# Performance work log

Hardware: AMD Instinct MI355X
Metric: run time of the kernel (lower is better)

Reference implementation:

```python
import jax, jax.numpy as jnp
import numpy as np

HID = 512; HH = HID // 2; INP = 1; OUT = 1
INH = int(HID * 0.3); EXC = HID - INH            # 153 / 359
N = 3 * HH + 2 * HID + INP                       # 1793 total units
ALM_EXC_START = 3 * HH + HID                      # start of ALM excitatory block
T_CONST = 0.1; SIGMA_REC = 0.01
B, T = 128, 300


def _np_masks():
    rng = np.random.default_rng(0)
    n_zeros = int(np.ceil(0.9 * HH))
    sparse = np.ones((HH, HH), np.float32)
    for c in range(HH):
        sparse[rng.permutation(HH)[:n_zeros], c] = 0.0
    alm2str = np.concatenate([np.ones((HH, EXC), np.float32), np.zeros((HH, INH), np.float32)], 1)
    thal2d1 = np.concatenate([np.ones((HH // 2, HID), np.float32), np.zeros((HH // 2, HID), np.float32)], 0)
    alm2d1 = 1.0 - thal2d1
    iti2d1 = np.concatenate([np.ones((HH // 2, INP), np.float32), np.zeros((HH // 2, INP), np.float32)], 0)
    alm_sign = np.concatenate([np.ones(EXC, np.float32), -np.ones(INH, np.float32)])  # alm2alm_D diagonal
    return sparse, alm2str, thal2d1, alm2d1, iti2d1, alm_sign

_SPARSE, _ALM2STR, _THAL2D1M, _ALM2D1M, _ITI2D1M, _ALMSIGN = [jnp.asarray(a) for a in _np_masks()]


def _clip(w):
    return jnp.clip(w, 1e-10, 1.0)               # F.hardtanh(w, 1e-10, 1)


def _build_W(d12d1_w, d12d2_w, d22d1_w, d22d2_w, d22stn_w, d12thal_w, stn2thal_w,
             thal2alm_w, alm2alm_w, thal2d1_w, thal2d2_w, alm2d1_w, alm2d2_w,
             inp_w_d1, inp_w_d2):
    z_ss = jnp.zeros((HH, HH)); z_sl = jnp.zeros((HH, HID))
    z_ls = jnp.zeros((HID, HH)); z_ll = jnp.zeros((HID, HID))
    z_si = jnp.zeros((HH, INP)); z_li = jnp.zeros((HID, INP))
    # striatal recurrence: sparse_mask * hardtanh(w) @ (-I)
    d12d1 = -(_SPARSE * _clip(d12d1_w)); d12d2 = -(_SPARSE * _clip(d12d2_w))
    d22d1 = -(_SPARSE * _clip(d22d1_w)); d22d2 = -(_SPARSE * _clip(d22d2_w))
    row_d1 = jnp.concatenate([d12d1, d22d1, z_ss, _THAL2D1M * _clip(thal2d1_w),
                              _ALM2D1M * _ALM2STR * _clip(alm2d1_w), _ITI2D1M * _clip(inp_w_d1)], 1)
    row_d2 = jnp.concatenate([d12d2, d22d2, z_ss, _clip(thal2d2_w),
                              _ALM2STR * _clip(alm2d2_w), _clip(inp_w_d2)], 1)
    row_stn = jnp.concatenate([z_ss, _clip(d22stn_w), z_ss, z_sl, z_sl, z_si], 1)
    row_thal = jnp.concatenate([_clip(d12thal_w), z_ls, -_clip(stn2thal_w), z_ll, z_ll, z_li], 1)  # stn2thal @ (-I)
    row_alm = jnp.concatenate([z_ls, z_ls, z_ls, _clip(thal2alm_w),
                               _clip(alm2alm_w) * _ALMSIGN[None, :], z_li], 1)      # alm2alm @ D (Dale)
    row_iti = jnp.zeros((INP, N))
    return jnp.concatenate([row_d1, row_d2, row_stn, row_thal, row_alm, row_iti], 0)


def setup_inputs() -> dict:
    key = jax.random.key(0)
    ks = jax.random.split(key, 24)
    u = lambda k, s: jax.random.uniform(k, s, jnp.float32) * 0.01   # uniform(0, 0.01) init
    return {
        "inp": jax.random.uniform(ks[0], (B, T, INP), jnp.float32),
        "cue_inp": jax.random.uniform(ks[1], (B, T, INP), jnp.float32),
        "inhib_stim": jnp.zeros((B, T, N), jnp.float32),
        "hn": jax.random.uniform(ks[2], (1, B, N), jnp.float32),
        "xn": jax.random.uniform(ks[3], (1, B, N), jnp.float32),
        "noise": jax.random.normal(ks[4], (B, T, N), jnp.float32),
        "d12d1_w": u(ks[5], (HH, HH)), "d12d2_w": u(ks[6], (HH, HH)),
        "d22d1_w": u(ks[7], (HH, HH)), "d22d2_w": u(ks[8], (HH, HH)),
        "d22stn_w": u(ks[9], (HH, HH)), "d12thal_w": u(ks[10], (HID, HH)),
        "stn2thal_w": u(ks[11], (HID, HH)), "thal2alm_w": u(ks[12], (HID, HID)),
        "alm2alm_w": u(ks[13], (HID, HID)), "thal2d1_w": u(ks[14], (HH, HID)),
        "thal2d2_w": u(ks[15], (HH, HID)), "alm2d1_w": u(ks[16], (HH, HID)),
        "alm2d2_w": u(ks[17], (HH, HID)), "inp_w_d1": u(ks[18], (HH, INP)),
        "inp_w_d2": u(ks[19], (HH, INP)), "out_w_alm": u(ks[20], (OUT, EXC)),
    }


def reference(inp, cue_inp, inhib_stim, hn, xn, noise,
              d12d1_w, d12d2_w, d22d1_w, d22d2_w, d22stn_w, d12thal_w, stn2thal_w,
              thal2alm_w, alm2alm_w, thal2d1_w, thal2d2_w, alm2d1_w, alm2d2_w,
              inp_w_d1, inp_w_d2, out_w_alm):
    W = _build_W(d12d1_w, d12d2_w, d22d1_w, d22d2_w, d22stn_w, d12thal_w, stn2thal_w,
                 thal2alm_w, alm2alm_w, thal2d1_w, thal2d2_w, alm2d1_w, alm2d2_w,
                 inp_w_d1, inp_w_d2)
    # tonic current: 0.1 everywhere except ITI units
    tonic = jnp.concatenate([0.1 * jnp.ones(N - INP, jnp.float32), jnp.zeros(INP, jnp.float32)])
    seq = (inhib_stim.swapaxes(0, 1),                 # [T, B, N]
           (inp + cue_inp).swapaxes(0, 1),            # [T, B, INP] -> injected into ITI units
           noise.swapaxes(0, 1))                      # [T, B, N]

    def step(carry, s):
        x, h = carry
        inh_t, iti_t, noise_t = s
        drive = h @ W.T + tonic + inh_t + SIGMA_REC * noise_t
        drive = drive.at[:, N - INP:].add(iti_t)
        x = x + T_CONST * (-x + drive)
        h = jax.nn.relu(x)
        out = h[:, ALM_EXC_START:ALM_EXC_START + EXC] @ out_w_alm.T
        return (x, h), (h, x, out)

    (_, _), (hs, xs, outs) = jax.lax.scan(step, (xn[0], hn[0]), seq)
    return hs.swapaxes(0, 1), xs.swapaxes(0, 1), outs.swapaxes(0, 1)
```

## Files before the change

### kernel.cpp

```cpp
#include <hip/hip_runtime.h>
#include <stdint.h>
#include <string.h>

#define NREAL 1793
#define NPAD  1824
#define NROWP 1808
#define WSTR  1832
#define NBLK  113
#define NGRP  2
#define TSTEPS 300
#define BATCH 128
#define XS_OFF 68851200
#define OUT_OFF 137702400
#define LOFF (16 * WSTR)
#define LOSCALE 4096.0f
#define LOINV  2.44140625e-4f

#define XLDR_IDX(g,x) (((g) * 8 + (x)) * 32)
#define XFLG_IDX(g,x) ((16 + (g) * 8 + (x)) * 32)
#define ASLOT(g,i)    (32 * 32 + (g) * 128 + (i))

typedef _Float16 half_t;
typedef __attribute__((ext_vector_type(8))) _Float16 half8;
typedef __attribute__((ext_vector_type(4))) float f32x4;
typedef __attribute__((ext_vector_type(4))) unsigned int uint4v;

__device__ __forceinline__ float clipw(float w) {
  return fminf(fmaxf(w, 1e-10f), 1.0f);
}

__device__ __forceinline__ void store_u32_llc(unsigned int* p, unsigned int v) {
  asm volatile("global_store_dword %0, %1, off sc0 sc1"
               :: "v"((unsigned long long)(uintptr_t)p), "v"(v)
               : "memory");
}
__device__ __forceinline__ void store_f32_llc(float* p, float v) {
  asm volatile("global_store_dword %0, %1, off sc0 sc1"
               :: "v"((unsigned long long)(uintptr_t)p), "v"(v)
               : "memory");
}

__device__ __forceinline__ float unpack_h(uint32_t p) {
  unsigned short uh = (unsigned short)(p & 0xffffu);
  unsigned short ul = (unsigned short)(p >> 16);
  half_t hh = *(half_t*)&uh;
  half_t hl = *(half_t*)&ul;
  return (float)hh + LOINV * (float)hl;
}

template<int LO0, int N0, int LO1, int N1, int LO2, int N2>
__device__ __forceinline__ void seg_mfma(const uint32_t* __restrict__ ap,
                                         const half_t* __restrict__ Wl, int wl_b,
                                         f32x4& acc0, f32x4& acc1, f32x4& acc2)
{
  constexpr int NC = N0 + N1 + N2;
  if (NC == 0) return;
  uint4v q0[NC ? NC : 1], q1[NC ? NC : 1];
  #pragma unroll
  for (int i = 0; i < NC; ++i) {
    const int kc = (i < N0) ? (LO0 + i)
                 : (i < N0 + N1) ? (LO1 + i - N0)
                 : (LO2 + i - N0 - N1);
    q0[i] = *(const uint4v*)(ap + kc * 32);
    q1[i] = *(const uint4v*)(ap + kc * 32 + 4);
  }
  #pragma unroll
  for (int i = 0; i < NC; ++i) {
    const int kc = (i < N0) ? (LO0 + i)
                 : (i < N0 + N1) ? (LO1 + i - N0)
                 : (LO2 + i - N0 - N1);
    uint4v uh, ul;
    uh.x = __builtin_amdgcn_perm(q0[i].y, q0[i].x, 0x05040100u);
    uh.y = __builtin_amdgcn_perm(q0[i].w, q0[i].z, 0x05040100u);
    uh.z = __builtin_amdgcn_perm(q1[i].y, q1[i].x, 0x05040100u);
    uh.w = __builtin_amdgcn_perm(q1[i].w, q1[i].z, 0x05040100u);
    ul.x = __builtin_amdgcn_perm(q0[i].y, q0[i].x, 0x07060302u);
    ul.y = __builtin_amdgcn_perm(q0[i].w, q0[i].z, 0x07060302u);
    ul.z = __builtin_amdgcn_perm(q1[i].y, q1[i].x, 0x07060302u);
    ul.w = __builtin_amdgcn_perm(q1[i].w, q1[i].z, 0x07060302u);
    union { uint4v u; half8 h; } ch, cl;
    ch.u = uh; cl.u = ul;
    half8 bvh = *(const half8*)&Wl[wl_b + kc * 32];
    half8 bvl = *(const half8*)&Wl[LOFF + wl_b + kc * 32];
    acc0 = __builtin_amdgcn_mfma_f32_16x16x32_f16(ch.h, bvh, acc0, 0, 0, 0);
    acc1 = __builtin_amdgcn_mfma_f32_16x16x32_f16(ch.h, bvl, acc1, 0, 0, 0);
    acc2 = __builtin_amdgcn_mfma_f32_16x16x32_f16(cl.h, bvh, acc2, 0, 0, 0);
  }
}

__global__ __launch_bounds__(256)
void build_w(const float* __restrict__ d12d1, const float* __restrict__ d12d2,
             const float* __restrict__ d22d1, const float* __restrict__ d22d2,
             const float* __restrict__ d22stn, const float* __restrict__ d12thal,
             const float* __restrict__ stn2thal, const float* __restrict__ thal2alm,
             const float* __restrict__ alm2alm, const float* __restrict__ thal2d1,
             const float* __restrict__ thal2d2, const float* __restrict__ alm2d1,
             const float* __restrict__ alm2d2, const float* __restrict__ inpw1,
             const float* __restrict__ inpw2, const unsigned int* __restrict__ mbits,
             half_t* __restrict__ W)
{
  int idx = blockIdx.x * 256 + threadIdx.x;
  if (idx >= NROWP * NPAD) return;
  int i = idx / NPAD, j = idx - (idx / NPAD) * NPAD;
  float v = 0.f;
  if (i < NREAL && j < NREAL) {
    if (i < 256) {
      if (j < 512) {
        int jj = j & 255;
        unsigned bit = (mbits[(i << 3) + (jj >> 5)] >> (jj & 31)) & 1u;
        float wv = (j < 256) ? d12d1[(i << 8) + jj] : d22d1[(i << 8) + jj];
        v = bit ? -clipw(wv) : 0.f;
      } else if (j < 768) {
      } else if (j < 1280) {
        if (i < 128) v = clipw(thal2d1[(i << 9) + (j - 768)]);
      } else if (j < 1792) {
        int jj = j - 1280;
        if (i >= 128 && jj < 359) v = clipw(alm2d1[(i << 9) + jj]);
      } else {
        if (i < 128) v = clipw(inpw1[i]);
      }
    } else if (i < 512) {
      int ii = i - 256;
      if (j < 512) {
        int jj = j & 255;
        unsigned bit = (mbits[(ii << 3) + (jj >> 5)] >> (jj & 31)) & 1u;
        float wv = (j < 256) ? d12d2[(ii << 8) + jj] : d22d2[(ii << 8) + jj];
        v = bit ? -clipw(wv) : 0.f;
      } else if (j < 768) {
      } else if (j < 1280) {
        v = clipw(thal2d2[(ii << 9) + (j - 768)]);
      } else if (j < 1792) {
        int jj = j - 1280;
        if (jj < 359) v = clipw(alm2d2[(ii << 9) + jj]);
      } else {
        v = clipw(inpw2[ii]);
      }
    } else if (i < 768) {
      int ii = i - 512;
      if (j >= 256 && j < 512) v = clipw(d22stn[(ii << 8) + (j - 256)]);
    } else if (i < 1280) {
      int ii = i - 768;
      if (j < 256) v = clipw(d12thal[(ii << 8) + j]);
      else if (j >= 512 && j < 768) v = -clipw(stn2thal[(ii << 8) + (j - 512)]);
    } else if (i < 1792) {
      int ii = i - 1280;
      if (j >= 768 && j < 1280) v = clipw(thal2alm[(ii << 9) + (j - 768)]);
      else if (j >= 1280) {
        int jj = j - 1280;
        v = clipw(alm2alm[(ii << 9) + jj]) * ((jj < 359) ? 1.f : -1.f);
      }
    }
  }
  half_t vh = (half_t)v;
  half_t vl = (half_t)((v - (float)vh) * LOSCALE);
  W[idx] = vh;
  W[(size_t)NROWP * NPAD + idx] = vl;
}

__global__ __launch_bounds__(256)
void init_h(const float* __restrict__ hn, uint32_t* __restrict__ hbuf)
{
  const size_t P4 = (size_t)BATCH * NPAD;
  int idx = blockIdx.x * 256 + threadIdx.x;
  if (idx >= BATCH * NPAD) return;
  int b = idx / NPAD, k = idx - b * NPAD;
  float v = (k < NREAL) ? hn[b * NREAL + k] : 0.f;
  half_t vh = (half_t)v;
  half_t vl = (half_t)((v - (float)vh) * LOSCALE);
  uint32_t hp = (uint32_t)(*(unsigned short*)&vh) |
                ((uint32_t)(*(unsigned short*)&vl) << 16);
  hbuf[idx]      = hp;
  hbuf[P4 + idx] = 0u;
}

__global__ __launch_bounds__(256, 1)
void rnn_step_all(const half_t* __restrict__ Wg, uint32_t* __restrict__ hbuf,
                  unsigned int* __restrict__ cnt,
                  const float* __restrict__ inp, const float* __restrict__ cue,
                  const float* __restrict__ inhib, const float* __restrict__ noise,
                  const float* __restrict__ xn, const float* __restrict__ outw,
                  float* __restrict__ dout)
{
  __shared__ __align__(16) half_t Wl[2 * 16 * WSTR];
  __shared__ unsigned int s_sync[2];
  const int tid = threadIdx.x;
  const int bid = blockIdx.x;
  const int g  = bid / NBLK;
  const int nb = bid - g * NBLK;
  const int r0 = nb * 16;
  const int bg = g * 64;
  const size_t P4 = (size_t)BATCH * NPAD;

  const int lane = tid & 63;
  const int w    = tid >> 6;
  const int n_i  = lane & 15;
  const int kq   = lane >> 4;
  const int row  = r0 + n_i;
  const bool valid = row < NREAL;
  const int b0 = bg + 16 * w + kq * 4;
  const int bA = bg + 16 * w + n_i;
  const int wl_b = n_i * WSTR + kq * 8;
  const bool is_outblk = (r0 == 512);
  const bool light = (r0 >= 512 && r0 < 1280) || (r0 == 1792);

  uint32_t xcc = 0;
  if (tid == 0) {
    asm volatile("s_getreg_b32 %0, hwreg(HW_REG_XCC_ID)" : "=s"(xcc));
    xcc &= 7u;
    unsigned int ldr = 0;
    if (light)
      ldr = (atomicCAS(&cnt[XLDR_IDX(g, xcc)], 0u, (uint32_t)bid + 1u) == 0u);
    s_sync[0] = xcc;
    s_sync[1] = ldr;
  }

  float inh[4], noi[4];
  #pragma unroll
  for (int r = 0; r < 4; ++r) {
    inh[r] = 0.f; noi[r] = 0.f;
    if (valid) {
      int ei = ((b0 + r) * TSTEPS) * NREAL + row;
      inh[r] = __builtin_nontemporal_load(&inhib[ei]);
      noi[r] = __builtin_nontemporal_load(&noise[ei]);
    }
  }

  for (int idx = tid; idx < 2 * 16 * (NPAD / 8); idx += 256) {
    int p   = idx / (16 * (NPAD / 8));
    int rem = idx - p * 16 * (NPAD / 8);
    int rr  = rem / (NPAD / 8);
    int cc  = (rem - rr * (NPAD / 8)) * 8;
    *(uint4v*)&Wl[p * LOFF + rr * WSTR + cc] =
        *(const uint4v*)&Wg[(size_t)p * NROWP * NPAD + (size_t)(r0 + rr) * NPAD + cc];
  }
  __syncthreads();

  if (tid == 0 && !light) {
    if (__hip_atomic_load(&cnt[XLDR_IDX(g, s_sync[0])], __ATOMIC_RELAXED,
                          __HIP_MEMORY_SCOPE_AGENT) == 0u)
      s_sync[1] = (atomicCAS(&cnt[XLDR_IDX(g, s_sync[0])], 0u,
                             (uint32_t)bid + 1u) == 0u);
  }
  __syncthreads();
  const uint32_t xcc_b  = s_sync[0];
  const bool     isldr  = (s_sync[1] != 0);
  const bool lead_wave  = isldr && (tid < 64);

  float xr[4];
  #pragma unroll
  for (int r = 0; r < 4; ++r)
    xr[r] = valid ? xn[(size_t)(b0 + r) * NREAL + row] : 0.f;

  const float tonic = (valid && row < 1792) ? 0.1f : 0.f;
  const bool is_iti = (row == 1792);

  const int ob    = bg + 16 * w + (lane >> 2);
  const int opart = lane & 3;
  const int ou0   = opart * 90;
  const int onu   = (opart == 3) ? 89 : 90;

  #pragma unroll 1
  for (int t = 0; t < TSTEPS; ++t) {
    const uint32_t* hr = hbuf + (size_t)(t & 1) * P4;
    uint32_t*       hw = hbuf + (size_t)((t & 1) ^ 1) * P4;

    float itv[4];
    #pragma unroll
    for (int r = 0; r < 4; ++r) {
      int bt = (b0 + r) * TSTEPS + t;
      itv[r] = is_iti ? (inp[bt] + cue[bt]) : 0.f;
    }

    const uint32_t* ap = hr + (size_t)bA * NPAD + kq * 8;
    f32x4 acc0 = {0.f, 0.f, 0.f, 0.f};
    f32x4 acc1 = {0.f, 0.f, 0.f, 0.f};
    f32x4 acc2 = {0.f, 0.f, 0.f, 0.f};

    if      (r0 < 128)  seg_mfma<0, 16, 24, 16, 56, 1>(ap, Wl, wl_b, acc0, acc1, acc2);
    else if (r0 < 256)  seg_mfma<0, 16, 40, 12,  0, 0>(ap, Wl, wl_b, acc0, acc1, acc2);
    else if (r0 < 512)  seg_mfma<0, 16, 24, 28, 56, 1>(ap, Wl, wl_b, acc0, acc1, acc2);
    else if (r0 < 768)  seg_mfma<8,  8,  0,  0,  0, 0>(ap, Wl, wl_b, acc0, acc1, acc2);
    else if (r0 < 1280) seg_mfma<0,  8, 16,  8,  0, 0>(ap, Wl, wl_b, acc0, acc1, acc2);
    else if (r0 < 1792) seg_mfma<24, 32, 0,  0,  0, 0>(ap, Wl, wl_b, acc0, acc1, acc2);

    #pragma unroll
    for (int r = 0; r < 4; ++r) {
      float drive = acc0[r] + LOINV * (acc1[r] + acc2[r])
                    + tonic + inh[r] + 0.01f * noi[r] + itv[r];
      float xv = xr[r] + 0.1f * (drive - xr[r]);
      float hv = fmaxf(xv, 0.f);
      xr[r] = xv;
      int bt = (b0 + r) * TSTEPS + t;
      if (valid) {
        int ei = bt * NREAL + row;
        store_f32_llc(&dout[ei], hv);
        store_f32_llc(&dout[XS_OFF + ei], xv);
      }
      half_t hh = (half_t)hv;
      half_t hl = (half_t)((hv - (float)hh) * LOSCALE);
      uint32_t hp = (uint32_t)(*(unsigned short*)&hh) |
                    ((uint32_t)(*(unsigned short*)&hl) << 16);
      store_u32_llc(&hw[(size_t)(b0 + r) * NPAD + row], hp);
    }

    if (is_outblk && t >= 1) {
      const uint32_t* hb = hr + (size_t)ob * NPAD + 1280 + ou0;
      float s = 0.f;
      #pragma unroll 10
      for (int i = 0; i < onu; ++i)
        s += unpack_h(hb[i]) * outw[ou0 + i];
      s += __shfl_xor(s, 1);
      s += __shfl_xor(s, 2);
      if (opart == 0)
        __builtin_nontemporal_store(s, &dout[OUT_OFF + ob * TSTEPS + (t - 1)]);
    }

    if (t + 1 < TSTEPS) {
      #pragma unroll
      for (int r = 0; r < 4; ++r) {
        if (valid) {
          int ei = ((b0 + r) * TSTEPS + (t + 1)) * NREAL + row;
          inh[r] = __builtin_nontemporal_load(&inhib[ei]);
          noi[r] = __builtin_nontemporal_load(&noise[ei]);
        }
      }
      const unsigned epoch = (unsigned)(t + 1);
      asm volatile("s_waitcnt vmcnt(8)" ::: "memory");
      __builtin_amdgcn_s_barrier();
      if (tid == 0)
        store_u32_llc(&cnt[ASLOT(g, nb)], epoch);
      if (lead_wave) {
        unsigned m;
        for (;;) {
          unsigned v0 = __hip_atomic_load(&cnt[ASLOT(g, lane)],
                                          __ATOMIC_RELAXED, __HIP_MEMORY_SCOPE_AGENT);
          unsigned v1 = 0xFFFFFFFFu;
          if (lane + 64 < NBLK)
            v1 = __hip_atomic_load(&cnt[ASLOT(g, lane + 64)],
                                   __ATOMIC_RELAXED, __HIP_MEMORY_SCOPE_AGENT);
          m = v0 < v1 ? v0 : v1;
          #pragma unroll
          for (int o = 32; o; o >>= 1) {
            unsigned mo = __shfl_xor(m, o);
            m = m < mo ? m : mo;
          }
          if (m >= epoch) break;
          __builtin_amdgcn_s_sleep(2);
        }
        if (lane == 0) {
          __builtin_amdgcn_fence(__ATOMIC_ACQUIRE, "agent");
          asm volatile("s_waitcnt vmcnt(0)" ::: "memory");
          __hip_atomic_store(&cnt[XFLG_IDX(g, xcc_b)], epoch,
                             __ATOMIC_RELAXED, __HIP_MEMORY_SCOPE_AGENT);
        }
      } else if (tid == 0) {
        while (__hip_atomic_load(&cnt[XFLG_IDX(g, xcc_b)], __ATOMIC_RELAXED,
                                 __HIP_MEMORY_SCOPE_AGENT) < epoch)
          __builtin_amdgcn_s_sleep(2);
        asm volatile("buffer_inv sc0" ::: "memory");
      }
      __builtin_amdgcn_s_barrier();
    }
  }

  asm volatile("s_waitcnt vmcnt(0)" ::: "memory");
  __builtin_amdgcn_s_barrier();
  if (tid == 0)
    store_u32_llc(&cnt[ASLOT(g, nb)], (unsigned)TSTEPS);
  if (lead_wave) {
    unsigned m;
    for (;;) {
      unsigned v0 = __hip_atomic_load(&cnt[ASLOT(g, lane)],
                                      __ATOMIC_RELAXED, __HIP_MEMORY_SCOPE_AGENT);
      unsigned v1 = 0xFFFFFFFFu;
      if (lane + 64 < NBLK)
        v1 = __hip_atomic_load(&cnt[ASLOT(g, lane + 64)],
                               __ATOMIC_RELAXED, __HIP_MEMORY_SCOPE_AGENT);
      m = v0 < v1 ? v0 : v1;
      #pragma unroll
      for (int o = 32; o; o >>= 1) {
        unsigned mo = __shfl_xor(m, o);
        m = m < mo ? m : mo;
      }
      if (m >= (unsigned)TSTEPS) break;
      __builtin_amdgcn_s_sleep(2);
    }
    if (lane == 0) {
      __builtin_amdgcn_fence(__ATOMIC_ACQUIRE, "agent");
      asm volatile("s_waitcnt vmcnt(0)" ::: "memory");
      __hip_atomic_store(&cnt[XFLG_IDX(g, xcc_b)], (unsigned)TSTEPS,
                         __ATOMIC_RELAXED, __HIP_MEMORY_SCOPE_AGENT);
    }
  } else if (is_outblk && tid == 0) {
    while (__hip_atomic_load(&cnt[XFLG_IDX(g, xcc_b)], __ATOMIC_RELAXED,
                             __HIP_MEMORY_SCOPE_AGENT) < (unsigned)TSTEPS)
      __builtin_amdgcn_s_sleep(2);
    asm volatile("buffer_inv sc0" ::: "memory");
  }
  if (is_outblk) {
    __builtin_amdgcn_s_barrier();
    const uint32_t* hr = hbuf + (size_t)(TSTEPS & 1) * P4;
    const uint32_t* hb = hr + (size_t)ob * NPAD + 1280 + ou0;
    float s = 0.f;
    #pragma unroll 10
    for (int i = 0; i < onu; ++i)
      s += unpack_h(hb[i]) * outw[ou0 + i];
    s += __shfl_xor(s, 1);
    s += __shfl_xor(s, 2);
    if (opart == 0)
      __builtin_nontemporal_store(s, &dout[OUT_OFF + ob * TSTEPS + (TSTEPS - 1)]);
  }
}

static void compute_sparse_mask(uint32_t* mb) {
  uint32_t pool[4];
  uint32_t hc = 0x43b0d7e5u;
  auto hashmix = [&hc](uint32_t value) -> uint32_t {
    value ^= hc; hc *= 0x931e8875u; value *= hc; value ^= value >> 16; return value;
  };
  auto mixf = [](uint32_t x, uint32_t y) -> uint32_t {
    uint32_t r = x * 0xca01f9ddu;
    r -= y * 0x4973f715u;
    r ^= r >> 16;
    return r;
  };
  for (int i = 0; i < 4; ++i) pool[i] = hashmix(0u);
  for (int s = 0; s < 4; ++s)
    for (int d = 0; d < 4; ++d)
      if (s != d) pool[d] = mixf(pool[d], hashmix(pool[s]));
  uint32_t st[8];
  uint32_t hb = 0x8b51f9ddu;
  for (int i = 0; i < 8; ++i) {
    uint32_t dv = pool[i & 3];
    dv ^= hb; hb *= 0x58f38dedu; dv *= hb; dv ^= dv >> 16;
    st[i] = dv;
  }
  uint64_t v64[4];
  for (int i = 0; i < 4; ++i) v64[i] = (uint64_t)st[2 * i] | ((uint64_t)st[2 * i + 1] << 32);
  typedef unsigned __int128 u128;
  const u128 MULT = ((u128)0x2360ed051fc65da4ULL << 64) | 0x4385df649fccf645ULL;
  u128 initstate = ((u128)v64[0] << 64) | v64[1];
  u128 initseq   = ((u128)v64[2] << 64) | v64[3];
  u128 state = 0, inc = (initseq << 1) | 1;
  state = state * MULT + inc;
  state += initstate;
  state = state * MULT + inc;
  bool has32 = false; uint32_t cached = 0;
  auto next64 = [&]() -> uint64_t {
    state = state * MULT + inc;
    uint64_t hi = (uint64_t)(state >> 64), lo = (uint64_t)state;
    unsigned rot = (unsigned)(state >> 122);
    uint64_t x = hi ^ lo;
    return (x >> rot) | (x << ((64 - rot) & 63));
  };
  auto next32 = [&]() -> uint32_t {
    if (has32) { has32 = false; return cached; }
    uint64_t v = next64();
    has32 = true; cached = (uint32_t)(v >> 32);
    return (uint32_t)v;
  };
  auto rinterval = [&](uint32_t mx) -> uint32_t {
    if (mx == 0) return 0;
    uint32_t mask = mx;
    mask |= mask >> 1; mask |= mask >> 2; mask |= mask >> 4;
    mask |= mask >> 8; mask |= mask >> 16;
    uint32_t value;
    do { value = next32() & mask; } while (value > mx);
    return value;
  };
  for (int i = 0; i < 256 * 8; ++i) mb[i] = 0xFFFFFFFFu;
  int perm[256];
  for (int c = 0; c < 256; ++c) {
    for (int i = 0; i < 256; ++i) perm[i] = i;
    for (int i = 255; i >= 1; --i) {
      uint32_t j = rinterval((uint32_t)i);
      int tmp = perm[i]; perm[i] = perm[j]; perm[j] = tmp;
    }
    for (int z = 0; z < 231; ++z)
      mb[perm[z] * 8 + (c >> 5)] &= ~(1u << (c & 31));
  }
}

extern "C" void kernel_launch(void* const* d_in, const int* in_sizes, int n_in,
                              void* d_out, int out_size, void* d_ws, size_t ws_size,
                              hipStream_t stream)
{
  (void)in_sizes; (void)n_in; (void)out_size; (void)ws_size;
  const float* inp   = (const float*)d_in[0];
  const float* cue   = (const float*)d_in[1];
  const float* inhib = (const float*)d_in[2];
  const float* hn    = (const float*)d_in[3];
  const float* xn    = (const float*)d_in[4];
  const float* noise = (const float*)d_in[5];
  const float* outw  = (const float*)d_in[21];
  float* dout = (float*)d_out;

  char* ws = (char*)d_ws;
  const size_t W_BYTES = (size_t)2 * NROWP * NPAD * sizeof(half_t);
  const size_t H_BYTES = (size_t)2 * BATCH * NPAD * 4;
  half_t*   W    = (half_t*)ws;
  uint32_t* hbuf = (uint32_t*)(ws + W_BYTES);
  unsigned int* mbits = (unsigned int*)(ws + W_BYTES + H_BYTES);
  unsigned int* cnt   = (unsigned int*)(ws + W_BYTES + H_BYTES + 16384);

  static uint32_t hmask[256 * 8];
  compute_sparse_mask(hmask);
  (void)hipMemcpyAsync(mbits, hmask, sizeof(hmask), hipMemcpyHostToDevice, stream);
  (void)hipMemsetAsync(cnt, 0, 16384, stream);

  build_w<<<(NROWP * NPAD + 255) / 256, 256, 0, stream>>>(
      (const float*)d_in[6],  (const float*)d_in[7],  (const float*)d_in[8],
      (const float*)d_in[9],  (const float*)d_in[10], (const float*)d_in[11],
      (const float*)d_in[12], (const float*)d_in[13], (const float*)d_in[14],
      (const float*)d_in[15], (const float*)d_in[16], (const float*)d_in[17],
      (const float*)d_in[18], (const float*)d_in[19], (const float*)d_in[20],
      mbits, W);
  init_h<<<(BATCH * NPAD + 255) / 256, 256, 0, stream>>>(hn, hbuf);

  void* args[] = {(void*)&W, (void*)&hbuf, (void*)&cnt, (void*)&inp, (void*)&cue,
                  (void*)&inhib, (void*)&noise, (void*)&xn, (void*)&outw, (void*)&dout};
  hipError_t err = hipLaunchCooperativeKernel(reinterpret_cast<void*>(rnn_step_all),
                                              dim3(NGRP * NBLK), dim3(256), args, 0, stream);
  if (err != hipSuccess) {
    rnn_step_all<<<dim3(NGRP * NBLK), dim3(256), 0, stream>>>(
        W, hbuf, cnt, inp, cue, inhib, noise, xn, outw, dout);
  }
}
```

Measured before the change: 4.196 ms.

## Replace per-XCC leader barrier with direct all-block polling of padded flags

Removes the two-level grid barrier, where one leader block per XCC polled all arrival slots and then released a per-XCC flag. Now every block's first wave polls all arrival counters directly. Each counter gets its own 128-byte-strided slot, and the poll sleep is shortened. The h/x output stores switch from sc0/sc1 LLC stores to nontemporal stores. This cuts one hop of latency per timestep, but every block now generates polling traffic on the shared counters.

```diff
diff --git a/kernel.cpp b/kernel.cpp
--- a/kernel.cpp
+++ b/kernel.cpp
@@ -16,9 +16,7 @@
 #define LOSCALE 4096.0f
 #define LOINV  2.44140625e-4f
 
-#define XLDR_IDX(g,x) (((g) * 8 + (x)) * 32)
-#define XFLG_IDX(g,x) ((16 + (g) * 8 + (x)) * 32)
-#define ASLOT(g,i)    (32 * 32 + (g) * 128 + (i))
+#define ASLOT(g,i)    (((g) * 128 + (i)) * 32)
 
 typedef _Float16 half_t;
 typedef __attribute__((ext_vector_type(8))) _Float16 half8;
@@ -30,11 +28,6 @@
 }
 
 __device__ __forceinline__ void store_u32_llc(unsigned int* p, unsigned int v) {
-  asm volatile("global_store_dword %0, %1, off sc0 sc1"
-               :: "v"((unsigned long long)(uintptr_t)p), "v"(v)
-               : "memory");
-}
-__device__ __forceinline__ void store_f32_llc(float* p, float v) {
   asm volatile("global_store_dword %0, %1, off sc0 sc1"
                :: "v"((unsigned long long)(uintptr_t)p), "v"(v)
                : "memory");
@@ -182,7 +175,6 @@
                   float* __restrict__ dout)
 {
   __shared__ __align__(16) half_t Wl[2 * 16 * WSTR];
-  __shared__ unsigned int s_sync[2];
   const int tid = threadIdx.x;
   const int bid = blockIdx.x;
   const int g  = bid / NBLK;
@@ -201,18 +193,7 @@
   const int bA = bg + 16 * w + n_i;
   const int wl_b = n_i * WSTR + kq * 8;
   const bool is_outblk = (r0 == 512);
-  const bool light = (r0 >= 512 && r0 < 1280) || (r0 == 1792);
-
-  uint32_t xcc = 0;
-  if (tid == 0) {
-    asm volatile("s_getreg_b32 %0, hwreg(HW_REG_XCC_ID)" : "=s"(xcc));
-    xcc &= 7u;
-    unsigned int ldr = 0;
-    if (light)
-      ldr = (atomicCAS(&cnt[XLDR_IDX(g, xcc)], 0u, (uint32_t)bid + 1u) == 0u);
-    s_sync[0] = xcc;
-    s_sync[1] = ldr;
-  }
+  const bool poll_wave = (tid < 64);
 
   float inh[4], noi[4];
   #pragma unroll
@@ -234,17 +215,6 @@
         *(const uint4v*)&Wg[(size_t)p * NROWP * NPAD + (size_t)(r0 + rr) * NPAD + cc];
   }
   __syncthreads();
-
-  if (tid == 0 && !light) {
-    if (__hip_atomic_load(&cnt[XLDR_IDX(g, s_sync[0])], __ATOMIC_RELAXED,
-                          __HIP_MEMORY_SCOPE_AGENT) == 0u)
-      s_sync[1] = (atomicCAS(&cnt[XLDR_IDX(g, s_sync[0])], 0u,
-                             (uint32_t)bid + 1u) == 0u);
-  }
-  __syncthreads();
-  const uint32_t xcc_b  = s_sync[0];
-  const bool     isldr  = (s_sync[1] != 0);
-  const bool lead_wave  = isldr && (tid < 64);
 
   float xr[4];
   #pragma unroll
@@ -293,8 +263,8 @@
       int bt = (b0 + r) * TSTEPS + t;
       if (valid) {
         int ei = bt * NREAL + row;
-        store_f32_llc(&dout[ei], hv);
-        store_f32_llc(&dout[XS_OFF + ei], xv);
+        __builtin_nontemporal_store(hv, &dout[ei]);
+        __builtin_nontemporal_store(xv, &dout[XS_OFF + ei]);
       }
       half_t hh = (half_t)hv;
       half_t hl = (half_t)((hv - (float)hh) * LOSCALE);
@@ -329,7 +299,7 @@
       __builtin_amdgcn_s_barrier();
       if (tid == 0)
         store_u32_llc(&cnt[ASLOT(g, nb)], epoch);
-      if (lead_wave) {
+      if (poll_wave) {
         unsigned m;
         for (;;) {
           unsigned v0 = __hip_atomic_load(&cnt[ASLOT(g, lane)],
@@ -345,19 +315,10 @@
             m = m < mo ? m : mo;
           }
           if (m >= epoch) break;
-          __builtin_amdgcn_s_sleep(2);
+          __builtin_amdgcn_s_sleep(1);
         }
-        if (lane == 0) {
-          __builtin_amdgcn_fence(__ATOMIC_ACQUIRE, "agent");
-          asm volatile("s_waitcnt vmcnt(0)" ::: "memory");
-          __hip_atomic_store(&cnt[XFLG_IDX(g, xcc_b)], epoch,
-                             __ATOMIC_RELAXED, __HIP_MEMORY_SCOPE_AGENT);
-        }
-      } else if (tid == 0) {
-        while (__hip_atomic_load(&cnt[XFLG_IDX(g, xcc_b)], __ATOMIC_RELAXED,
-                                 __HIP_MEMORY_SCOPE_AGENT) < epoch)
-          __builtin_amdgcn_s_sleep(2);
-        asm volatile("buffer_inv sc0" ::: "memory");
+        __builtin_amdgcn_fence(__ATOMIC_ACQUIRE, "agent");
+        asm volatile("s_waitcnt vmcnt(0)" ::: "memory");
       }
       __builtin_amdgcn_s_barrier();
     }
@@ -367,37 +328,28 @@
   __builtin_amdgcn_s_barrier();
   if (tid == 0)
     store_u32_llc(&cnt[ASLOT(g, nb)], (unsigned)TSTEPS);
-  if (lead_wave) {
-    unsigned m;
-    for (;;) {
-      unsigned v0 = __hip_atomic_load(&cnt[ASLOT(g, lane)],
-                                      __ATOMIC_RELAXED, __HIP_MEMORY_SCOPE_AGENT);
-      unsigned v1 = 0xFFFFFFFFu;
-      if (lane + 64 < NBLK)
-        v1 = __hip_atomic_load(&cnt[ASLOT(g, lane + 64)],
-                               __ATOMIC_RELAXED, __HIP_MEMORY_SCOPE_AGENT);
-      m = v0 < v1 ? v0 : v1;
-      #pragma unroll
-      for (int o = 32; o; o >>= 1) {
-        unsigned mo = __shfl_xor(m, o);
-        m = m < mo ? m : mo;
-      }
-      if (m >= (unsigned)TSTEPS) break;
-      __builtin_amdgcn_s_sleep(2);
-    }
-    if (lane == 0) {
+  if (is_outblk) {
+    if (poll_wave) {
+      unsigned m;
+      for (;;) {
+        unsigned v0 = __hip_atomic_load(&cnt[ASLOT(g, lane)],
+                                        __ATOMIC_RELAXED, __HIP_MEMORY_SCOPE_AGENT);
+        unsigned v1 = 0xFFFFFFFFu;
+        if (lane + 64 < NBLK)
+          v1 = __hip_atomic_load(&cnt[ASLOT(g, lane + 64)],
+                                 __ATOMIC_RELAXED, __HIP_MEMORY_SCOPE_AGENT);
+        m = v0 < v1 ? v0 : v1;
+        #pragma unroll
+        for (int o = 32; o; o >>= 1) {
+          unsigned mo = __shfl_xor(m, o);
+          m = m < mo ? m : mo;
+        }
+        if (m >= (unsigned)TSTEPS) break;
+        __builtin_amdgcn_s_sleep(1);
+      }
       __builtin_amdgcn_fence(__ATOMIC_ACQUIRE, "agent");
       asm volatile("s_waitcnt vmcnt(0)" ::: "memory");
-      __hip_atomic_store(&cnt[XFLG_IDX(g, xcc_b)], (unsigned)TSTEPS,
-                         __ATOMIC_RELAXED, __HIP_MEMORY_SCOPE_AGENT);
-    }
-  } else if (is_outblk && tid == 0) {
-    while (__hip_atomic_load(&cnt[XFLG_IDX(g, xcc_b)], __ATOMIC_RELAXED,
-                             __HIP_MEMORY_SCOPE_AGENT) < (unsigned)TSTEPS)
-      __builtin_amdgcn_s_sleep(2);
-    asm volatile("buffer_inv sc0" ::: "memory");
-  }
-  if (is_outblk) {
+    }
     __builtin_amdgcn_s_barrier();
     const uint32_t* hr = hbuf + (size_t)(TSTEPS & 1) * P4;
     const uint32_t* hb = hr + (size_t)ob * NPAD + 1280 + ou0;
@@ -501,12 +453,12 @@
   half_t*   W    = (half_t*)ws;
   uint32_t* hbuf = (uint32_t*)(ws + W_BYTES);
   unsigned int* mbits = (unsigned int*)(ws + W_BYTES + H_BYTES);
-  unsigned int* cnt   = (unsigned int*)(ws + W_BYTES + H_BYTES + 16384);
+  unsigned int* cnt   = (unsigned int*)(ws + W_BYTES + H_BYTES + 32768);
 
   static uint32_t hmask[256 * 8];
   compute_sparse_mask(hmask);
   (void)hipMemcpyAsync(mbits, hmask, sizeof(hmask), hipMemcpyHostToDevice, stream);
-  (void)hipMemsetAsync(cnt, 0, 16384, stream);
+  (void)hipMemsetAsync(cnt, 0, 32768, stream);
 
   build_w<<<(NROWP * NPAD + 255) / 256, 256, 0, stream>>>(
       (const float*)d_in[6],  (const float*)d_in[7],  (const float*)d_in[8],
```

New measurement: 4.143 ms. About the same (-1.3%).
